# Kernel tuning notes

Hardware: AMD Instinct MI355X
Metric: run time of the kernel (lower is better)

## Reference

```python
import jax, jax.numpy as jnp
import numpy as np

C, N, T, I = 8, 1024, 8, 64   # num_confs, num_nodes, num_node_types, in_feat
H, F = 4, 64                  # num_heads, out_feat
DEG = 16
E = C * N * DEG
NEG_SLOPE = 0.2


def setup_inputs() -> dict:
    key = jax.random.key(0)
    k1, k2, k3, k4, k5, k6 = jax.random.split(key, 6)
    node_feats = jax.random.normal(k1, (C, N, T, I), dtype=jnp.float32)
    # edges are within-conformer: flat index = c*N + local
    conf = jnp.repeat(jnp.arange(C), N * DEG)
    src = conf * N + jax.random.randint(k2, (E,), 0, N)
    dst = conf * N + jax.random.randint(k3, (E,), 0, N)
    edge_idx = jnp.stack([src, dst]).astype(jnp.int64)
    # parameters (xavier-normal-like scaling)
    fc = jax.random.normal(k4, (T, I, F * H), dtype=jnp.float32) * np.sqrt(2.0 / (I + F * H))
    attn_src = jax.random.normal(k5, (1, H, F * T), dtype=jnp.float32) * np.sqrt(2.0 / (F * T))
    attn_dst = jax.random.normal(k6, (1, H, F * T), dtype=jnp.float32) * np.sqrt(2.0 / (F * T))
    return {"edge_idx": edge_idx, "node_feats": node_feats, "fc": fc,
            "attn_src": attn_src, "attn_dst": attn_dst}


def _forward(node_feats, fc, attn_src, attn_dst, edge_idx):
    C_, N_, T_, I_ = node_feats.shape
    H_ = attn_src.shape[1]
    F_ = attn_src.shape[2] // T_
    h = node_feats.reshape(C_ * N_, T_, I_)
    # per-type FC projection: (C*N, T, H*F)
    feat = jnp.einsum('bji,jik->bjk', h, fc)
    # replicate the exact reshape/permute sequence of the torch code
    feat = feat.reshape(C_, N_, T_, F_ * H_).transpose(0, 2, 1, 3)          # (C,T,N,F*H)
    feat = feat.reshape(C_, N_, T_, H_, F_).transpose(0, 1, 3, 2, 4)        # (C,N,H,T,F)
    feat = feat.reshape(C_ * N_, H_, T_ * F_)                               # (C*N,H,T*F)
    # endpoint masks: nodes appearing as src/dst get 1, others 0
    src_present = jnp.zeros((C_ * N_,), feat.dtype).at[edge_idx[0]].set(1.0)
    dst_present = jnp.zeros((C_ * N_,), feat.dtype).at[edge_idx[1]].set(1.0)
    feat_src = feat * src_present[:, None, None]
    feat_dst = feat * dst_present[:, None, None]
    a_src = jnp.clip(feat_src * attn_src, -1e9, 1e9).reshape(C_, N_, H_, T_ * F_).sum(-1)
    a_dst = jnp.clip(feat_dst * attn_dst, -1e9, 1e9).reshape(C_, N_, H_, T_ * F_).sum(-1)
    a = a_src[:, :, None, :] + a_dst[:, None, :, :]   # (C, src, dst, H)
    a = jnp.where(a >= 0, a, NEG_SLOPE * a)            # leaky_relu
    # dense per-conformer adjacency from flat edge indices
    c_s, i_s = edge_idx[0] // N_, edge_idx[0] % N_
    j_d = edge_idx[1] % N_
    adj = jnp.zeros((C_, N_, N_), bool).at[c_s, i_s, j_d].set(True)
    logits = jnp.where(adj[..., None], a, jnp.asarray(-1e9, a.dtype))
    attn = jax.nn.softmax(logits, axis=1)              # normalize over sources per dst
    attn = jnp.where(adj[..., None], attn, 0.0)
    feat_v = feat.reshape(C_, N_, H_, T_ * F_)
    out = jnp.einsum('cijh,cihf->cjhf', attn, feat_v)  # (C,N,H,T*F)
    out = out.mean(axis=2).reshape(C_, N_, T_, F_)     # (C,N,T,F)
    return out, attn


def reference(edge_idx, node_feats, fc, attn_src, attn_dst):
    return _forward(node_feats, fc, attn_src, attn_dst, edge_idx)
```

## Files before the change

### kernel.cpp

```cpp
#include <hip/hip_runtime.h>

typedef short  bf16x8 __attribute__((ext_vector_type(8)));
typedef float  f32x4  __attribute__((ext_vector_type(4)));
typedef unsigned u32x4 __attribute__((ext_vector_type(4)));

#define CC 8
#define NN 1024
#define TT 8
#define II 64
#define HH 4
#define FF 64
#define EE (CC*NN*16)
#define KK 256
#define MAXD 64

static const size_t OUT_ELEMS  = (size_t)CC*NN*TT*FF;
static const size_t ATTN_ELEMS = (size_t)CC*NN*NN*HH;

static const size_t PG_OFF   = 0;
static const size_t ASRC_OFF = 33554432;
static const size_t ADST_OFF = ASRC_OFF + 131072;
static const size_t ADJ_OFF  = ADST_OFF + 131072;
static const size_t DEG_OFF  = ADJ_OFF + 1048576;
static const size_t LIST_OFF = DEG_OFF + 32768;
static const size_t FCT_OFF  = LIST_OFF + 1048576;

static __device__ inline unsigned short f2bf(float x) {
    union { float f; unsigned u; } q; q.f = x;
    unsigned r = q.u + 0x7fffu + ((q.u >> 16) & 1u);
    return (unsigned short)(r >> 16);
}
static __device__ inline float bf2f(unsigned short u) {
    return __uint_as_float(((unsigned)u) << 16);
}

__global__ __launch_bounds__(256) void k0_prep(const float* __restrict__ fc,
                                               unsigned short* __restrict__ fcT,
                                               uint4* __restrict__ zbase) {
    int bx = blockIdx.x;
    int tid = threadIdx.x;
    if (bx < 66) {
        uint4 z = make_uint4(0u, 0u, 0u, 0u);
        uint4* p = zbase + (size_t)bx*1024;
        #pragma unroll
        for (int r = 0; r < 4; ++r) p[r*256 + tid] = z;
    } else {
        int b = bx - 66;
        int t = b >> 2, ib = (b & 3) << 4;
        __shared__ unsigned short ls[256][17];
        #pragma unroll
        for (int r = 0; r < 16; ++r)
            ls[tid][r] = f2bf(fc[(size_t)(t*64 + ib + r)*KK + tid]);
        __syncthreads();
        int ii = tid & 15, k0 = tid >> 4;
        #pragma unroll
        for (int it = 0; it < 16; ++it) {
            int k = it*16 + k0;
            fcT[(size_t)t*16384 + (size_t)k*64 + ib + ii] = ls[k][ii];
        }
    }
}

__global__ __launch_bounds__(256) void k1_mfma(const float* __restrict__ nf,
                                               const unsigned short* __restrict__ fcT,
                                               const float* __restrict__ avs,
                                               const float* __restrict__ avd,
                                               unsigned short* __restrict__ Pg,
                                               float* __restrict__ a_src,
                                               float* __restrict__ a_dst,
                                               const int* __restrict__ ei,
                                               unsigned* __restrict__ adj,
                                               int* __restrict__ deg,
                                               unsigned short* __restrict__ lists,
                                               u32x4* __restrict__ attnz) {
    int bxg = blockIdx.x;
    int tid = threadIdx.x;

    if (bxg >= 1536) {
        u32x4 z = (u32x4)(0u);
        u32x4* p = attnz + (size_t)(bxg - 1536)*1024;
        #pragma unroll
        for (int r = 0; r < 4; ++r)
            __builtin_nontemporal_store(z, &p[r*256 + tid]);
        return;
    }
    if (bxg >= 1024) {
        int e = (bxg - 1024)*256 + tid;
        int s = ei[e];
        int d = ei[EE + e];
        int c = s >> 10, i = s & 1023, j = d & 1023;
        int cj = (c << 10) + j;
        unsigned bit = 1u << (i & 31);
        unsigned old = atomicOr(&adj[(size_t)cj*32 + (i >> 5)], bit);
        if (!(old & bit)) {
            int pos = atomicAdd(&deg[cj], 1);
            if (pos < MAXD) lists[(size_t)cj*MAXD + pos] = (unsigned short)i;
        }
        return;
    }

    __shared__ unsigned short stg[8*2048];
    __shared__ float avsL[2048];
    __shared__ float avdL[2048];
    int bx = bxg;
    int c = bx & 7, t = (bx >> 3) & 7, tile = bx >> 6;
    int w = tid >> 6, lane = tid & 63;
    int col = lane & 15, g = lane >> 4;

    for (int l = tid; l < 2048; l += 256) {
        int t2 = l & 7, cl = (l >> 3) & 15, ctl = (l >> 7) & 3, h = l >> 9;
        int si = h*512 + t2*64 + ctl*16 + cl;
        avsL[l] = avs[si];
        avdL[l] = avd[si];
    }

    int row = tile*64 + w*16 + col;
    const float* ap = nf + ((size_t)(c*NN + row)*TT + t)*II + g*8;
    bf16x8 afr[2];
    #pragma unroll
    for (int ks = 0; ks < 2; ++ks) {
        float4 x = *(const float4*)(ap + ks*32);
        float4 y = *(const float4*)(ap + ks*32 + 4);
        afr[ks][0] = (short)f2bf(x.x); afr[ks][1] = (short)f2bf(x.y);
        afr[ks][2] = (short)f2bf(x.z); afr[ks][3] = (short)f2bf(x.w);
        afr[ks][4] = (short)f2bf(y.x); afr[ks][5] = (short)f2bf(y.y);
        afr[ks][6] = (short)f2bf(y.z); afr[ks][7] = (short)f2bf(y.w);
    }

    const unsigned short* bp = fcT + (size_t)t*256*64 + col*64 + g*8;
    f32x4 acc[16];
    #pragma unroll
    for (int ct = 0; ct < 16; ++ct) {
        bf16x8 b0 = *(const bf16x8*)(bp + (size_t)ct*16*64);
        bf16x8 b1 = *(const bf16x8*)(bp + (size_t)ct*16*64 + 32);
        f32x4 a; a[0] = 0.f; a[1] = 0.f; a[2] = 0.f; a[3] = 0.f;
        a = __builtin_amdgcn_mfma_f32_16x16x32_bf16(afr[0], b0, a, 0, 0, 0);
        a = __builtin_amdgcn_mfma_f32_16x16x32_bf16(afr[1], b1, a, 0, 0, 0);
        acc[ct] = a;
    }

    int nd = w*2 + (g >> 1);
    int t2b = (g & 1)*4;
    #pragma unroll
    for (int ctl = 0; ctl < 4; ++ctl) {
        int f2 = ctl*16 + col;
        #pragma unroll
        for (int v = 0; v < 4; ++v) {
            unsigned u0 = (unsigned)f2bf(acc[ctl     ][v]) | ((unsigned)f2bf(acc[ 4+ctl][v]) << 16);
            unsigned u1 = (unsigned)f2bf(acc[ 8+ctl][v]) | ((unsigned)f2bf(acc[12+ctl][v]) << 16);
            *(uint2*)&stg[nd*2048 + (t2b + v)*256 + f2*4] = make_uint2(u0, u1);
        }
    }

    __syncthreads();

    #pragma unroll
    for (int h = 0; h < 4; ++h) {
        float s = 0.f, d = 0.f;
        #pragma unroll
        for (int ctl = 0; ctl < 4; ++ctl) {
            float4 wS = *(const float4*)&avsL[((h*4 + ctl)*16 + col)*8 + t2b];
            float4 wD = *(const float4*)&avdL[((h*4 + ctl)*16 + col)*8 + t2b];
            f32x4 a = acc[h*4 + ctl];
            s += a[0]*wS.x + a[1]*wS.y + a[2]*wS.z + a[3]*wS.w;
            d += a[0]*wD.x + a[1]*wD.y + a[2]*wD.z + a[3]*wD.w;
        }
        #pragma unroll
        for (int m = 1; m <= 16; m <<= 1) { s += __shfl_xor(s, m); d += __shfl_xor(d, m); }
        if ((lane & 31) == 0) {
            int n2 = t*128 + tile*8 + w*2 + (lane >> 5);
            a_src[(size_t)(c*NN + n2)*HH + h] = s;
            a_dst[(size_t)(c*NN + n2)*HH + h] = d;
        }
    }

    {
        size_t gb = ((size_t)(c*NN) + t*128 + tile*8)*2048;
        const uint4* s4 = (const uint4*)stg;
        uint4* g4 = (uint4*)(Pg + gb);
        for (int l = tid; l < 2048; l += 256) g4[l] = s4[l];
    }
}

static __device__ inline void fma8(uint4 pv, float4 wv, float& a0, float& a1) {
    a0 += wv.x*bf2f((unsigned short)(pv.x & 0xffffu))
        + wv.y*bf2f((unsigned short)(pv.x >> 16))
        + wv.z*bf2f((unsigned short)(pv.y & 0xffffu))
        + wv.w*bf2f((unsigned short)(pv.y >> 16));
    a1 += wv.x*bf2f((unsigned short)(pv.z & 0xffffu))
        + wv.y*bf2f((unsigned short)(pv.z >> 16))
        + wv.z*bf2f((unsigned short)(pv.w & 0xffffu))
        + wv.w*bf2f((unsigned short)(pv.w >> 16));
}

__global__ __launch_bounds__(256) void k5_attn(const unsigned short* __restrict__ Pg,
                                               const float* __restrict__ a_src,
                                               const float* __restrict__ a_dst,
                                               const int* __restrict__ deg,
                                               const unsigned short* __restrict__ lists,
                                               float* __restrict__ attn_out,
                                               float* __restrict__ out) {
    __shared__ unsigned short L[MAXD];
    __shared__ __align__(16) float attL[MAXD][4];
    int bx = blockIdx.x;
    int c = bx & 7, j = bx >> 3;
    int cb = c << 10;
    int cj = cb + j;
    int tid = threadIdx.x;

    int n = deg[cj]; if (n > MAXD) n = MAXD;
    int nn = (n + 3) & ~3;

    if (tid < n) L[tid] = lists[(size_t)cj*MAXD + tid];
    if (tid >= n && tid < nn) {
        L[tid] = 0;
        *(f32x4*)attL[tid] = (f32x4)(0.f);
    }
    __syncthreads();

    int h = tid >> 6, lane = tid & 63;
    float adv = a_dst[(size_t)cj*4 + h];

    float m = -1e30f;
    for (int e = lane; e < n; e += 64) {
        float z = a_src[(size_t)(cb + L[e])*4 + h] + adv;
        z = (z < 0.f) ? 0.2f*z : z;
        attL[e][h] = z;
        m = fmaxf(m, z);
    }
    #pragma unroll
    for (int mm = 32; mm; mm >>= 1) m = fmaxf(m, __shfl_xor(m, mm));
    float ssum = 0.f;
    for (int e = lane; e < n; e += 64) {
        float ez = __expf(attL[e][h] - m);
        attL[e][h] = ez;
        ssum += ez;
    }
    #pragma unroll
    for (int mm = 32; mm; mm >>= 1) ssum += __shfl_xor(ssum, mm);
    float inv = (n > 0) ? 1.f / ssum : 0.f;
    for (int e = lane; e < n; e += 64) attL[e][h] *= inv;
    __syncthreads();

    if (tid < n) {
        int i = L[tid];
        f32x4 sv = *(const f32x4*)attL[tid];
        __builtin_nontemporal_store(sv, (f32x4*)&attn_out[((size_t)(cb + i)*NN + j)*4]);
    }

    float acc0 = 0.f, acc1 = 0.f, acc2 = 0.f, acc3 = 0.f;
    const unsigned short* pgBase = Pg + (size_t)cb*2048 + tid*8;
    for (int e0 = 0; e0 < nn; e0 += 4) {
        uint4 p0 = *(const uint4*)(pgBase + (size_t)L[e0+0]*2048);
        uint4 p1 = *(const uint4*)(pgBase + (size_t)L[e0+1]*2048);
        uint4 p2 = *(const uint4*)(pgBase + (size_t)L[e0+2]*2048);
        uint4 p3 = *(const uint4*)(pgBase + (size_t)L[e0+3]*2048);
        float4 w0 = *(const float4*)attL[e0+0];
        float4 w1 = *(const float4*)attL[e0+1];
        float4 w2 = *(const float4*)attL[e0+2];
        float4 w3 = *(const float4*)attL[e0+3];
        fma8(p0, w0, acc0, acc1);
        fma8(p1, w1, acc2, acc3);
        fma8(p2, w2, acc0, acc1);
        fma8(p3, w3, acc2, acc3);
    }
    float2 o = make_float2((acc0 + acc2)*0.25f, (acc1 + acc3)*0.25f);
    __builtin_nontemporal_store(o.x, &out[(size_t)cj*512 + tid*2]);
    __builtin_nontemporal_store(o.y, &out[(size_t)cj*512 + tid*2 + 1]);
}

extern "C" void kernel_launch(void* const* d_in, const int* in_sizes, int n_in,
                              void* d_out, int out_size, void* d_ws, size_t ws_size,
                              hipStream_t stream) {
    const int*   ei   = (const int*)d_in[0];
    const float* nf   = (const float*)d_in[1];
    const float* fc   = (const float*)d_in[2];
    const float* avs  = (const float*)d_in[3];
    const float* avd  = (const float*)d_in[4];

    float* out      = (float*)d_out;
    float* attn_out = out + OUT_ELEMS;

    char* ws = (char*)d_ws;
    unsigned short* Pg      = (unsigned short*)(ws + PG_OFF);
    float*          a_src_w = (float*)(ws + ASRC_OFF);
    float*          a_dst_w = (float*)(ws + ADST_OFF);
    unsigned*       adjw    = (unsigned*)(ws + ADJ_OFF);
    int*            degw    = (int*)(ws + DEG_OFF);
    unsigned short* listw   = (unsigned short*)(ws + LIST_OFF);
    unsigned short* fcTw    = (unsigned short*)(ws + FCT_OFF);

    k0_prep <<<98, 256, 0, stream>>>(fc, fcTw, (uint4*)(ws + ADJ_OFF));
    k1_mfma <<<9728, 256, 0, stream>>>(nf, fcTw, avs, avd, Pg, a_src_w, a_dst_w,
                                       ei, adjw, degw, listw, (u32x4*)attn_out);
    k5_attn <<<CC*NN, 256, 0, stream>>>(Pg, a_src_w, a_dst_w, degw, listw,
                                        attn_out, out);
}
```

Baseline: 93.26 us.

## Interleave fused-kernel block roles and map one wavefront per destination node

The fused k1 kernel now interleaves its three block roles (MFMA projection, adjacency build, attention zeroing) in a 2:1:16 pattern, so compute, atomics and zero-stores run together across the grid instead of in sequential block ranges. The k5 attention kernel is restructured so each wavefront handles one destination node, computing all four heads' softmax with wave shuffles in registers and no block-level barriers. Each lane now accumulates eight outputs per neighbor row, and block count is reduced four-fold. This trades LDS and syncthreads overhead for more registers and serial work per lane.

```diff
diff --git a/kernel.cpp b/kernel.cpp
--- a/kernel.cpp
+++ b/kernel.cpp
@@ -75,17 +75,19 @@
                                                u32x4* __restrict__ attnz) {
     int bxg = blockIdx.x;
     int tid = threadIdx.x;
-
-    if (bxg >= 1536) {
+    int q = bxg / 19;
+    int r = bxg - q*19;
+
+    if (r >= 3) {
         u32x4 z = (u32x4)(0u);
-        u32x4* p = attnz + (size_t)(bxg - 1536)*1024;
-        #pragma unroll
-        for (int r = 0; r < 4; ++r)
-            __builtin_nontemporal_store(z, &p[r*256 + tid]);
+        u32x4* p = attnz + (size_t)(q*16 + (r - 3))*1024;
+        #pragma unroll
+        for (int rr = 0; rr < 4; ++rr)
+            __builtin_nontemporal_store(z, &p[rr*256 + tid]);
         return;
     }
-    if (bxg >= 1024) {
-        int e = (bxg - 1024)*256 + tid;
+    if (r == 2) {
+        int e = q*256 + tid;
         int s = ei[e];
         int d = ei[EE + e];
         int c = s >> 10, i = s & 1023, j = d & 1023;
@@ -102,8 +104,8 @@
     __shared__ unsigned short stg[8*2048];
     __shared__ float avsL[2048];
     __shared__ float avdL[2048];
-    int bx = bxg;
-    int c = bx & 7, t = (bx >> 3) & 7, tile = bx >> 6;
+    int mb = q*2 + r;
+    int c = mb & 7, t = (mb >> 3) & 7, tile = mb >> 6;
     int w = tid >> 6, lane = tid & 63;
     int col = lane & 15, g = lane >> 4;
 
@@ -200,73 +202,95 @@
                                                const unsigned short* __restrict__ lists,
                                                float* __restrict__ attn_out,
                                                float* __restrict__ out) {
-    __shared__ unsigned short L[MAXD];
-    __shared__ __align__(16) float attL[MAXD][4];
-    int bx = blockIdx.x;
+    __shared__ __align__(16) float wL[4][64][4];
+    int wid = threadIdx.x >> 6;
+    int lane = threadIdx.x & 63;
+    int bx = blockIdx.x*4 + wid;
     int c = bx & 7, j = bx >> 3;
     int cb = c << 10;
     int cj = cb + j;
-    int tid = threadIdx.x;
 
     int n = deg[cj]; if (n > MAXD) n = MAXD;
-    int nn = (n + 3) & ~3;
-
-    if (tid < n) L[tid] = lists[(size_t)cj*MAXD + tid];
-    if (tid >= n && tid < nn) {
-        L[tid] = 0;
-        *(f32x4*)attL[tid] = (f32x4)(0.f);
-    }
-    __syncthreads();
-
-    int h = tid >> 6, lane = tid & 63;
-    float adv = a_dst[(size_t)cj*4 + h];
-
-    float m = -1e30f;
-    for (int e = lane; e < n; e += 64) {
-        float z = a_src[(size_t)(cb + L[e])*4 + h] + adv;
-        z = (z < 0.f) ? 0.2f*z : z;
-        attL[e][h] = z;
-        m = fmaxf(m, z);
-    }
-    #pragma unroll
-    for (int mm = 32; mm; mm >>= 1) m = fmaxf(m, __shfl_xor(m, mm));
-    float ssum = 0.f;
-    for (int e = lane; e < n; e += 64) {
-        float ez = __expf(attL[e][h] - m);
-        attL[e][h] = ez;
-        ssum += ez;
-    }
-    #pragma unroll
-    for (int mm = 32; mm; mm >>= 1) ssum += __shfl_xor(ssum, mm);
-    float inv = (n > 0) ? 1.f / ssum : 0.f;
-    for (int e = lane; e < n; e += 64) attL[e][h] *= inv;
-    __syncthreads();
-
-    if (tid < n) {
-        int i = L[tid];
-        f32x4 sv = *(const f32x4*)attL[tid];
-        __builtin_nontemporal_store(sv, (f32x4*)&attn_out[((size_t)(cb + i)*NN + j)*4]);
-    }
-
-    float acc0 = 0.f, acc1 = 0.f, acc2 = 0.f, acc3 = 0.f;
-    const unsigned short* pgBase = Pg + (size_t)cb*2048 + tid*8;
-    for (int e0 = 0; e0 < nn; e0 += 4) {
-        uint4 p0 = *(const uint4*)(pgBase + (size_t)L[e0+0]*2048);
-        uint4 p1 = *(const uint4*)(pgBase + (size_t)L[e0+1]*2048);
-        uint4 p2 = *(const uint4*)(pgBase + (size_t)L[e0+2]*2048);
-        uint4 p3 = *(const uint4*)(pgBase + (size_t)L[e0+3]*2048);
-        float4 w0 = *(const float4*)attL[e0+0];
-        float4 w1 = *(const float4*)attL[e0+1];
-        float4 w2 = *(const float4*)attL[e0+2];
-        float4 w3 = *(const float4*)attL[e0+3];
-        fma8(p0, w0, acc0, acc1);
-        fma8(p1, w1, acc2, acc3);
-        fma8(p2, w2, acc0, acc1);
-        fma8(p3, w3, acc2, acc3);
-    }
-    float2 o = make_float2((acc0 + acc2)*0.25f, (acc1 + acc3)*0.25f);
-    __builtin_nontemporal_store(o.x, &out[(size_t)cj*512 + tid*2]);
-    __builtin_nontemporal_store(o.y, &out[(size_t)cj*512 + tid*2 + 1]);
+    bool valid = lane < n;
+    int i = valid ? (int)lists[(size_t)cj*MAXD + lane] : 0;
+
+    float4 adv = *(const float4*)&a_dst[(size_t)cj*4];
+    float4 z4;
+    if (valid) {
+        float4 as = *(const float4*)&a_src[(size_t)(cb + i)*4];
+        z4.x = as.x + adv.x; z4.x = (z4.x < 0.f) ? 0.2f*z4.x : z4.x;
+        z4.y = as.y + adv.y; z4.y = (z4.y < 0.f) ? 0.2f*z4.y : z4.y;
+        z4.z = as.z + adv.z; z4.z = (z4.z < 0.f) ? 0.2f*z4.z : z4.z;
+        z4.w = as.w + adv.w; z4.w = (z4.w < 0.f) ? 0.2f*z4.w : z4.w;
+    } else {
+        z4 = make_float4(-1e30f, -1e30f, -1e30f, -1e30f);
+    }
+    float4 mx = z4;
+    #pragma unroll
+    for (int mm = 32; mm; mm >>= 1) {
+        mx.x = fmaxf(mx.x, __shfl_xor(mx.x, mm));
+        mx.y = fmaxf(mx.y, __shfl_xor(mx.y, mm));
+        mx.z = fmaxf(mx.z, __shfl_xor(mx.z, mm));
+        mx.w = fmaxf(mx.w, __shfl_xor(mx.w, mm));
+    }
+    float4 ez = make_float4(0.f, 0.f, 0.f, 0.f);
+    if (valid) {
+        ez.x = __expf(z4.x - mx.x);
+        ez.y = __expf(z4.y - mx.y);
+        ez.z = __expf(z4.z - mx.z);
+        ez.w = __expf(z4.w - mx.w);
+    }
+    float4 sm = ez;
+    #pragma unroll
+    for (int mm = 32; mm; mm >>= 1) {
+        sm.x += __shfl_xor(sm.x, mm);
+        sm.y += __shfl_xor(sm.y, mm);
+        sm.z += __shfl_xor(sm.z, mm);
+        sm.w += __shfl_xor(sm.w, mm);
+    }
+    float4 w4 = make_float4(0.f, 0.f, 0.f, 0.f);
+    if (valid) {
+        w4.x = ez.x / sm.x; w4.y = ez.y / sm.y;
+        w4.z = ez.z / sm.z; w4.w = ez.w / sm.w;
+        f32x4 sv; sv[0] = w4.x; sv[1] = w4.y; sv[2] = w4.z; sv[3] = w4.w;
+        __builtin_nontemporal_store(sv,
+            (f32x4*)&attn_out[((size_t)(cb + i)*NN + j)*4]);
+    }
+    *(float4*)wL[wid][lane] = w4;
+
+    float a0 = 0.f, a1 = 0.f, a2 = 0.f, a3 = 0.f;
+    float a4 = 0.f, a5 = 0.f, a6 = 0.f, a7 = 0.f;
+    const unsigned short* rowc = Pg + (size_t)cb*2048 + lane*8;
+    int nn2 = (n + 1) & ~1;
+    for (int e = 0; e < nn2; e += 2) {
+        int ia = __shfl(i, e);
+        int ib = __shfl(i, e + 1);
+        float4 wa = *(const float4*)wL[wid][e];
+        float4 wb = *(const float4*)wL[wid][e + 1 < 64 ? e + 1 : 63];
+        const unsigned short* ra = rowc + (size_t)ia*2048;
+        const unsigned short* rb = rowc + (size_t)ib*2048;
+        uint4 pa0 = *(const uint4*)(ra);
+        uint4 pa1 = *(const uint4*)(ra + 512);
+        uint4 pa2 = *(const uint4*)(ra + 1024);
+        uint4 pa3 = *(const uint4*)(ra + 1536);
+        uint4 pb0 = *(const uint4*)(rb);
+        uint4 pb1 = *(const uint4*)(rb + 512);
+        uint4 pb2 = *(const uint4*)(rb + 1024);
+        uint4 pb3 = *(const uint4*)(rb + 1536);
+        fma8(pa0, wa, a0, a1); fma8(pa1, wa, a2, a3);
+        fma8(pa2, wa, a4, a5); fma8(pa3, wa, a6, a7);
+        fma8(pb0, wb, a0, a1); fma8(pb1, wb, a2, a3);
+        fma8(pb2, wb, a4, a5); fma8(pb3, wb, a6, a7);
+    }
+    size_t ob = (size_t)cj*512 + lane*2;
+    __builtin_nontemporal_store(a0*0.25f, &out[ob]);
+    __builtin_nontemporal_store(a1*0.25f, &out[ob + 1]);
+    __builtin_nontemporal_store(a2*0.25f, &out[ob + 128]);
+    __builtin_nontemporal_store(a3*0.25f, &out[ob + 129]);
+    __builtin_nontemporal_store(a4*0.25f, &out[ob + 256]);
+    __builtin_nontemporal_store(a5*0.25f, &out[ob + 257]);
+    __builtin_nontemporal_store(a6*0.25f, &out[ob + 384]);
+    __builtin_nontemporal_store(a7*0.25f, &out[ob + 385]);
 }
 
 extern "C" void kernel_launch(void* const* d_in, const int* in_sizes, int n_in,
@@ -293,6 +317,6 @@
     k0_prep <<<98, 256, 0, stream>>>(fc, fcTw, (uint4*)(ws + ADJ_OFF));
     k1_mfma <<<9728, 256, 0, stream>>>(nf, fcTw, avs, avd, Pg, a_src_w, a_dst_w,
                                        ei, adjw, degw, listw, (u32x4*)attn_out);
-    k5_attn <<<CC*NN, 256, 0, stream>>>(Pg, a_src_w, a_dst_w, degw, listw,
-                                        attn_out, out);
-}
+    k5_attn <<<CC*NN/4, 256, 0, stream>>>(Pg, a_src_w, a_dst_w, degw, listw,
+                                          attn_out, out);
+}
```

After: 120.6 us. +29.3%, slower.

## Zero only non-edge attention entries in k5 using transposed adjacency bitmap

Applied to the files above, without the earlier changes.

The attention output used to be fully zeroed in k1 and then the edge entries were overwritten in k5. Now k1 builds a transposed adjacency bitmap, and extra blocks in k5 write zeros only where no edge exists, so those entries are written once and never twice. The zeroing also moves off the projection kernel's grid into the attention kernel, where it can overlap with the gather work. The aggregation loop is also unrolled from 4 to 8 edges per iteration, which costs an extra atomicOr per edge and more padding work.

```diff
diff --git a/kernel.cpp b/kernel.cpp
--- a/kernel.cpp
+++ b/kernel.cpp
@@ -21,7 +21,8 @@
 static const size_t ASRC_OFF = 33554432;
 static const size_t ADST_OFF = ASRC_OFF + 131072;
 static const size_t ADJ_OFF  = ADST_OFF + 131072;
-static const size_t DEG_OFF  = ADJ_OFF + 1048576;
+static const size_t ADJT_OFF = ADJ_OFF + 1048576;
+static const size_t DEG_OFF  = ADJT_OFF + 1048576;
 static const size_t LIST_OFF = DEG_OFF + 32768;
 static const size_t FCT_OFF  = LIST_OFF + 1048576;
 
@@ -39,13 +40,13 @@
                                                uint4* __restrict__ zbase) {
     int bx = blockIdx.x;
     int tid = threadIdx.x;
-    if (bx < 66) {
+    if (bx < 130) {
         uint4 z = make_uint4(0u, 0u, 0u, 0u);
         uint4* p = zbase + (size_t)bx*1024;
         #pragma unroll
         for (int r = 0; r < 4; ++r) p[r*256 + tid] = z;
     } else {
-        int b = bx - 66;
+        int b = bx - 130;
         int t = b >> 2, ib = (b & 3) << 4;
         __shared__ unsigned short ls[256][17];
         #pragma unroll
@@ -70,26 +71,19 @@
                                                float* __restrict__ a_dst,
                                                const int* __restrict__ ei,
                                                unsigned* __restrict__ adj,
+                                               unsigned* __restrict__ adjT,
                                                int* __restrict__ deg,
-                                               unsigned short* __restrict__ lists,
-                                               u32x4* __restrict__ attnz) {
+                                               unsigned short* __restrict__ lists) {
     int bxg = blockIdx.x;
     int tid = threadIdx.x;
 
-    if (bxg >= 1536) {
-        u32x4 z = (u32x4)(0u);
-        u32x4* p = attnz + (size_t)(bxg - 1536)*1024;
-        #pragma unroll
-        for (int r = 0; r < 4; ++r)
-            __builtin_nontemporal_store(z, &p[r*256 + tid]);
-        return;
-    }
     if (bxg >= 1024) {
         int e = (bxg - 1024)*256 + tid;
         int s = ei[e];
         int d = ei[EE + e];
         int c = s >> 10, i = s & 1023, j = d & 1023;
         int cj = (c << 10) + j;
+        atomicOr(&adjT[((size_t)((c << 10) + i))*32 + (j >> 5)], 1u << (j & 31));
         unsigned bit = 1u << (i & 31);
         unsigned old = atomicOr(&adj[(size_t)cj*32 + (i >> 5)], bit);
         if (!(old & bit)) {
@@ -198,18 +192,36 @@
                                                const float* __restrict__ a_dst,
                                                const int* __restrict__ deg,
                                                const unsigned short* __restrict__ lists,
+                                               const unsigned* __restrict__ adjT,
                                                float* __restrict__ attn_out,
                                                float* __restrict__ out) {
+    int bxg = blockIdx.x;
+    int tid = threadIdx.x;
+
+    if (bxg >= CC*NN) {
+        int idx = bxg - CC*NN;
+        int c = idx & 7, i = idx >> 3;
+        const unsigned* aw = adjT + (size_t)((c << 10) + i)*32;
+        f32x4 z = (f32x4)(0.f);
+        float* rowp = attn_out + (size_t)((c << 10) + i)*4096;
+        #pragma unroll
+        for (int r2 = 0; r2 < 4; ++r2) {
+            int jj = r2*256 + tid;
+            if (!((aw[jj >> 5] >> (jj & 31)) & 1u))
+                __builtin_nontemporal_store(z, (f32x4*)&rowp[jj*4]);
+        }
+        return;
+    }
+
     __shared__ unsigned short L[MAXD];
     __shared__ __align__(16) float attL[MAXD][4];
-    int bx = blockIdx.x;
+    int bx = bxg;
     int c = bx & 7, j = bx >> 3;
     int cb = c << 10;
     int cj = cb + j;
-    int tid = threadIdx.x;
 
     int n = deg[cj]; if (n > MAXD) n = MAXD;
-    int nn = (n + 3) & ~3;
+    int nn = (n + 7) & ~7;
 
     if (tid < n) L[tid] = lists[(size_t)cj*MAXD + tid];
     if (tid >= n && tid < nn) {
@@ -250,19 +262,31 @@
 
     float acc0 = 0.f, acc1 = 0.f, acc2 = 0.f, acc3 = 0.f;
     const unsigned short* pgBase = Pg + (size_t)cb*2048 + tid*8;
-    for (int e0 = 0; e0 < nn; e0 += 4) {
+    for (int e0 = 0; e0 < nn; e0 += 8) {
         uint4 p0 = *(const uint4*)(pgBase + (size_t)L[e0+0]*2048);
         uint4 p1 = *(const uint4*)(pgBase + (size_t)L[e0+1]*2048);
         uint4 p2 = *(const uint4*)(pgBase + (size_t)L[e0+2]*2048);
         uint4 p3 = *(const uint4*)(pgBase + (size_t)L[e0+3]*2048);
+        uint4 p4 = *(const uint4*)(pgBase + (size_t)L[e0+4]*2048);
+        uint4 p5 = *(const uint4*)(pgBase + (size_t)L[e0+5]*2048);
+        uint4 p6 = *(const uint4*)(pgBase + (size_t)L[e0+6]*2048);
+        uint4 p7 = *(const uint4*)(pgBase + (size_t)L[e0+7]*2048);
         float4 w0 = *(const float4*)attL[e0+0];
         float4 w1 = *(const float4*)attL[e0+1];
         float4 w2 = *(const float4*)attL[e0+2];
         float4 w3 = *(const float4*)attL[e0+3];
+        float4 w4 = *(const float4*)attL[e0+4];
+        float4 w5 = *(const float4*)attL[e0+5];
+        float4 w6 = *(const float4*)attL[e0+6];
+        float4 w7 = *(const float4*)attL[e0+7];
         fma8(p0, w0, acc0, acc1);
         fma8(p1, w1, acc2, acc3);
         fma8(p2, w2, acc0, acc1);
         fma8(p3, w3, acc2, acc3);
+        fma8(p4, w4, acc0, acc1);
+        fma8(p5, w5, acc2, acc3);
+        fma8(p6, w6, acc0, acc1);
+        fma8(p7, w7, acc2, acc3);
     }
     float2 o = make_float2((acc0 + acc2)*0.25f, (acc1 + acc3)*0.25f);
     __builtin_nontemporal_store(o.x, &out[(size_t)cj*512 + tid*2]);
@@ -286,13 +310,14 @@
     float*          a_src_w = (float*)(ws + ASRC_OFF);
     float*          a_dst_w = (float*)(ws + ADST_OFF);
     unsigned*       adjw    = (unsigned*)(ws + ADJ_OFF);
+    unsigned*       adjTw   = (unsigned*)(ws + ADJT_OFF);
     int*            degw    = (int*)(ws + DEG_OFF);
     unsigned short* listw   = (unsigned short*)(ws + LIST_OFF);
     unsigned short* fcTw    = (unsigned short*)(ws + FCT_OFF);
 
-    k0_prep <<<98, 256, 0, stream>>>(fc, fcTw, (uint4*)(ws + ADJ_OFF));
-    k1_mfma <<<9728, 256, 0, stream>>>(nf, fcTw, avs, avd, Pg, a_src_w, a_dst_w,
-                                       ei, adjw, degw, listw, (u32x4*)attn_out);
-    k5_attn <<<CC*NN, 256, 0, stream>>>(Pg, a_src_w, a_dst_w, degw, listw,
-                                        attn_out, out);
-}
+    k0_prep <<<162, 256, 0, stream>>>(fc, fcTw, (uint4*)(ws + ADJ_OFF));
+    k1_mfma <<<1536, 256, 0, stream>>>(nf, fcTw, avs, avd, Pg, a_src_w, a_dst_w,
+                                       ei, adjw, adjTw, degw, listw);
+    k5_attn <<<2*CC*NN, 256, 0, stream>>>(Pg, a_src_w, a_dst_w, degw, listw,
+                                          adjTw, attn_out, out);
+}
```

Result: slower. 112.3 us (+20.4%).
